# Optimization experiments

Hardware: AMD Instinct MI355X
Metric: run time of the kernel (lower is better)

Reference implementation:

```python
import jax, jax.numpy as jnp
import numpy as np

N_NODES = 100000
N_EDGES = 2500000


def setup_inputs() -> dict:
    key = jax.random.key(0)
    ks = jax.random.split(key, 6)
    x = jax.random.normal(ks[0], (N_NODES, 2), dtype=jnp.float32)
    edge_index = jax.random.randint(ks[1], (2, N_EDGES), 0, N_NODES, dtype=jnp.int32)
    # SAGEConv(2, 32): lin_l applied to mean-aggregated neighbors (carries bias),
    # lin_r applied to root features (no bias) -- PyG defaults.
    W_l1 = jax.random.normal(ks[2], (2, 32), dtype=jnp.float32) * 0.5
    W_r1 = jax.random.normal(ks[3], (2, 32), dtype=jnp.float32) * 0.5
    b1 = jnp.zeros((32,), jnp.float32)
    # SAGEConv(32, 2)
    W_l2 = jax.random.normal(ks[4], (32, 2), dtype=jnp.float32) * 0.1
    W_r2 = jax.random.normal(ks[5], (32, 2), dtype=jnp.float32) * 0.1
    b2 = jnp.zeros((2,), jnp.float32)
    return dict(x=x, edge_index=edge_index, W_l1=W_l1, W_r1=W_r1, b1=b1,
                W_l2=W_l2, W_r2=W_r2, b2=b2)


def _sage_conv(x, src, dst, deg_inv, W_l, W_r, b):
    # mean aggregation of source-node features at destination nodes
    summed = jax.ops.segment_sum(x[src], dst, num_segments=N_NODES)  # [N, F]
    agg = summed * deg_inv  # scatter-mean; isolated nodes get 0
    return agg @ W_l + x @ W_r + b


def reference(x, edge_index, W_l1, W_r1, b1, W_l2, W_r2, b2):
    src, dst = edge_index[0], edge_index[1]
    ones = jnp.ones((src.shape[0],), x.dtype)
    deg = jax.ops.segment_sum(ones, dst, num_segments=N_NODES)
    deg_inv = (1.0 / jnp.maximum(deg, 1.0))[:, None]  # [N, 1]
    h = jax.nn.relu(_sage_conv(x, src, dst, deg_inv, W_l1, W_r1, b1))
    out = _sage_conv(h, src, dst, deg_inv, W_l2, W_r2, b2)
    return jax.nn.log_softmax(out, axis=1)
```

## Files before the change

### kernel.cpp

```cpp
#include <hip/hip_runtime.h>

#define N_NODES 100000
#define N_EDGES 2500000
#define SBBITS 11
#define SBSZ 2048
#define NSB 49
#define SB 512
#define EPB 4883
#define TOT (NSB * SB)
#define P1B 25
#define M 16
#define AGG_GRID (NSB * M)


typedef unsigned int u32;
typedef unsigned long long u64;

__global__ void hist_k(const int* __restrict__ ei, u32* __restrict__ histG) {
    __shared__ u32 hl[NSB * 8];
    int t = threadIdx.x, b = blockIdx.x;
    for (int k = t; k < NSB * 8; k += 256) hl[k] = 0;
    __syncthreads();
    int e0 = b * EPB, e1 = min(e0 + EPB, N_EDGES);
    int r = t & 7;
    for (int e = e0 + t; e < e1; e += 256) {
        u32 dst = (u32)ei[N_EDGES + e];
        atomicAdd(&hl[(dst >> SBBITS) * 8 + r], 1u);
    }
    __syncthreads();
    for (int k = t; k < NSB; k += 256) {
        u32 s = 0;
#pragma unroll
        for (int j = 0; j < 8; ++j) s += hl[k * 8 + j];
        histG[k * SB + b] = s;
    }
}

__global__ void scan_p1(const u32* __restrict__ histG, u32* __restrict__ blockSum) {
    __shared__ u32 red[256];
    int t = threadIdx.x;
    int base = blockIdx.x * 1024;
    u32 s = 0;
#pragma unroll
    for (int j = 0; j < 4; ++j) {
        int idx = base + t * 4 + j;
        if (idx < TOT) s += histG[idx];
    }
    red[t] = s;
    __syncthreads();
    for (int off = 128; off > 0; off >>= 1) {
        if (t < off) red[t] += red[t + off];
        __syncthreads();
    }
    if (t == 0) blockSum[blockIdx.x] = red[0];
}

__global__ void scan_p2(const u32* __restrict__ blockSum, u32* __restrict__ blockBase) {
    __shared__ u32 ts[256];
    int t = threadIdx.x;
    u32 v[4];
    u32 s = 0;
#pragma unroll
    for (int j = 0; j < 4; ++j) {
        int idx = t * 4 + j;
        v[j] = (idx < P1B) ? blockSum[idx] : 0u;
        s += v[j];
    }
    ts[t] = s;
    __syncthreads();
    for (int off = 1; off < 256; off <<= 1) {
        u32 add = (t >= off) ? ts[t - off] : 0u;
        __syncthreads();
        ts[t] += add;
        __syncthreads();
    }
    u32 run = (t > 0) ? ts[t - 1] : 0u;
#pragma unroll
    for (int j = 0; j < 4; ++j) {
        int idx = t * 4 + j;
        if (idx < P1B) blockBase[idx] = run;
        run += v[j];
    }
}

__global__ void scan_p3(u32* histG, const u32* __restrict__ blockBase) {
    __shared__ u32 ts[256];
    int t = threadIdx.x;
    int base = blockIdx.x * 1024;
    u32 v[4];
    u32 s = 0;
#pragma unroll
    for (int j = 0; j < 4; ++j) {
        int idx = base + t * 4 + j;
        v[j] = (idx < TOT) ? histG[idx] : 0u;
        s += v[j];
    }
    ts[t] = s;
    __syncthreads();
    for (int off = 1; off < 256; off <<= 1) {
        u32 add = (t >= off) ? ts[t - off] : 0u;
        __syncthreads();
        ts[t] += add;
        __syncthreads();
    }
    u32 run = ((t > 0) ? ts[t - 1] : 0u) + blockBase[blockIdx.x];
#pragma unroll
    for (int j = 0; j < 4; ++j) {
        int idx = base + t * 4 + j;
        if (idx < TOT) histG[idx] = run;
        run += v[j];
    }
}

__global__ void scatter_k(const int* __restrict__ ei, const u32* __restrict__ histG,
                          u32* __restrict__ sortedE) {
    __shared__ u32 pos[NSB];
    int t = threadIdx.x, b = blockIdx.x;
    if (t < NSB) pos[t] = histG[t * SB + b];
    __syncthreads();
    int e0 = b * EPB, e1 = min(e0 + EPB, N_EDGES);
    for (int e = e0 + t; e < e1; e += 256) {
        u32 src = (u32)ei[e];
        u32 dst = (u32)ei[N_EDGES + e];
        u32 sb = dst >> SBBITS;
        u32 slot = atomicAdd(&pos[sb], 1u);
        sortedE[slot] = ((dst & (SBSZ - 1u)) << 17) | src;
    }
}

__global__ void agg1_k(const u32* __restrict__ sortedE, const u32* __restrict__ histG,
                       const float* __restrict__ x, u32* __restrict__ PART) {
    __shared__ u32 cntL[SBSZ], fxL[SBSZ], fyL[SBSZ];
    int t = threadIdx.x;
    u32 sb = blockIdx.x / M, m = blockIdx.x % M;
    for (int j = t; j < SBSZ; j += 256) { cntL[j] = 0; fxL[j] = 0; fyL[j] = 0; }
    __syncthreads();

    u32 s0 = histG[sb * SB];
    u32 s1 = (sb + 1 < NSB) ? histG[(sb + 1) * SB] : N_EDGES;
    u32 len = s1 - s0;
    u32 a = s0 + len * m / M;
    u32 bEnd = s0 + len * (m + 1) / M;
    const float2* x2 = (const float2*)x;

    u32 idx = a + t;
    while (idx + 256 < bEnd) {
        u32 p0 = sortedE[idx], p1 = sortedE[idx + 256];
        float2 v0 = x2[p0 & 0x1FFFFu];
        float2 v1 = x2[p1 & 0x1FFFFu];
        u32 l0 = p0 >> 17, l1 = p1 >> 17;
        atomicAdd(&cntL[l0], 1u);
        atomicAdd(&fxL[l0], (u32)((v0.x + 16.0f) * 65536.0f + 0.5f));
        atomicAdd(&fyL[l0], (u32)((v0.y + 16.0f) * 65536.0f + 0.5f));
        atomicAdd(&cntL[l1], 1u);
        atomicAdd(&fxL[l1], (u32)((v1.x + 16.0f) * 65536.0f + 0.5f));
        atomicAdd(&fyL[l1], (u32)((v1.y + 16.0f) * 65536.0f + 0.5f));
        idx += 512;
    }
    if (idx < bEnd) {
        u32 p = sortedE[idx];
        float2 v = x2[p & 0x1FFFFu];
        u32 l = p >> 17;
        atomicAdd(&cntL[l], 1u);
        atomicAdd(&fxL[l], (u32)((v.x + 16.0f) * 65536.0f + 0.5f));
        atomicAdd(&fyL[l], (u32)((v.y + 16.0f) * 65536.0f + 0.5f));
    }
    __syncthreads();

    u32 base = blockIdx.x * (3 * SBSZ);
    for (int j = t; j < SBSZ; j += 256) {
        PART[base + j] = cntL[j];
        PART[base + SBSZ + j] = fxL[j];
        PART[base + 2 * SBSZ + j] = fyL[j];
    }
}

__global__ void reduce1_node1(const u32* __restrict__ PART, const float* __restrict__ x,
                              const float* __restrict__ Wl1, const float* __restrict__ Wr1,
                              const float* __restrict__ b1,
                              const float* __restrict__ Wl2, const float* __restrict__ Wr2,
                              u64* __restrict__ ench2, float2* __restrict__ hrG,
                              float* __restrict__ degG) {
    __shared__ float sWl1[64], sWr1[64], sb1[32], sWl2[64], sWr2[64];
    int t = threadIdx.x;
    if (t < 64) { sWl1[t] = Wl1[t]; sWr1[t] = Wr1[t]; sWl2[t] = Wl2[t]; sWr2[t] = Wr2[t]; }
    if (t >= 64 && t < 96) sb1[t - 64] = b1[t - 64];
    __syncthreads();

    int i = blockIdx.x * 256 + t;
    if (i >= N_NODES) return;
    u32 sb = (u32)i >> SBBITS, j = (u32)i & (SBSZ - 1u);

    u32 cnt = 0, fx = 0, fy = 0;
#pragma unroll
    for (int m = 0; m < M; ++m) {
        u32 base = (sb * M + m) * (3 * SBSZ);
        cnt += PART[base + j];
        fx += PART[base + SBSZ + j];
        fy += PART[base + 2 * SBSZ + j];
    }

    float fc = (float)cnt;
    float dinv = 1.0f / fmaxf(fc, 1.0f);
    float ax = (float)(int)(fx - cnt * 1048576u) * (1.0f / 65536.0f) * dinv;
    float ay = (float)(int)(fy - cnt * 1048576u) * (1.0f / 65536.0f) * dinv;
    float2 xv = ((const float2*)x)[i];

    float h2a = 0.f, h2b = 0.f, hra = 0.f, hrb = 0.f;
#pragma unroll
    for (int f = 0; f < 32; ++f) {
        float h = ax * sWl1[f] + ay * sWl1[32 + f] + xv.x * sWr1[f] + xv.y * sWr1[32 + f] + sb1[f];
        h = fmaxf(h, 0.0f);
        h2a += h * sWl2[2 * f];
        h2b += h * sWl2[2 * f + 1];
        hra += h * sWr2[2 * f];
        hrb += h * sWr2[2 * f + 1];
    }
    u32 ex = (u32)((h2a + 2048.0f) * 4096.0f + 0.5f);
    u32 ey = (u32)((h2b + 2048.0f) * 4096.0f + 0.5f);
    ench2[i] = ((u64)ey << 32) | (u64)ex;
    hrG[i] = make_float2(hra, hrb);
    degG[i] = fc;
}

__global__ void agg2_k(const u32* __restrict__ sortedE, const u32* __restrict__ histG,
                       const u64* __restrict__ ench2, u32* __restrict__ PART2) {
    __shared__ u32 gxL[SBSZ], gyL[SBSZ];
    int t = threadIdx.x;
    u32 sb = blockIdx.x / M, m = blockIdx.x % M;
    for (int j = t; j < SBSZ; j += 256) { gxL[j] = 0; gyL[j] = 0; }
    __syncthreads();

    u32 s0 = histG[sb * SB];
    u32 s1 = (sb + 1 < NSB) ? histG[(sb + 1) * SB] : N_EDGES;
    u32 len = s1 - s0;
    u32 a = s0 + len * m / M;
    u32 bEnd = s0 + len * (m + 1) / M;

    u32 idx = a + t;
    while (idx + 256 < bEnd) {
        u32 p0 = sortedE[idx], p1 = sortedE[idx + 256];
        u64 e0 = ench2[p0 & 0x1FFFFu];
        u64 e1 = ench2[p1 & 0x1FFFFu];
        u32 l0 = p0 >> 17, l1 = p1 >> 17;
        atomicAdd(&gxL[l0], (u32)e0);
        atomicAdd(&gyL[l0], (u32)(e0 >> 32));
        atomicAdd(&gxL[l1], (u32)e1);
        atomicAdd(&gyL[l1], (u32)(e1 >> 32));
        idx += 512;
    }
    if (idx < bEnd) {
        u32 p = sortedE[idx];
        u64 e = ench2[p & 0x1FFFFu];
        u32 l = p >> 17;
        atomicAdd(&gxL[l], (u32)e);
        atomicAdd(&gyL[l], (u32)(e >> 32));
    }
    __syncthreads();

    u32 base = blockIdx.x * (2 * SBSZ);
    for (int j = t; j < SBSZ; j += 256) {
        PART2[base + j] = gxL[j];
        PART2[base + SBSZ + j] = gyL[j];
    }
}

__global__ void reduce2_node2(const u32* __restrict__ PART2, const float2* __restrict__ hrG,
                              const float* __restrict__ degG, const float* __restrict__ b2,
                              float* __restrict__ out) {
    int i = blockIdx.x * 256 + threadIdx.x;
    if (i >= N_NODES) return;
    u32 sb = (u32)i >> SBBITS, j = (u32)i & (SBSZ - 1u);

    u32 gx = 0, gy = 0;
#pragma unroll
    for (int m = 0; m < M; ++m) {
        u32 base = (sb * M + m) * (2 * SBSZ);
        gx += PART2[base + j];
        gy += PART2[base + SBSZ + j];
    }

    float fc = degG[i];
    u32 c = (u32)fc;
    float dinv = 1.0f / fmaxf(fc, 1.0f);
    float sx = (float)(int)(gx - c * 8388608u) * (1.0f / 4096.0f) * dinv;
    float sy = (float)(int)(gy - c * 8388608u) * (1.0f / 4096.0f) * dinv;
    float2 hv = hrG[i];
    float o0 = sx + hv.x + b2[0];
    float o1 = sy + hv.y + b2[1];
    float mx = fmaxf(o0, o1);
    float e0 = expf(o0 - mx);
    float e1 = expf(o1 - mx);
    float lse = logf(e0 + e1);
    ((float2*)out)[i] = make_float2(o0 - mx - lse, o1 - mx - lse);
}

extern "C" void kernel_launch(void* const* d_in, const int* in_sizes, int n_in,
                              void* d_out, int out_size, void* d_ws, size_t ws_size,
                              hipStream_t stream) {
    const float* x   = (const float*)d_in[0];
    const int*   ei  = (const int*)d_in[1];
    const float* Wl1 = (const float*)d_in[2];
    const float* Wr1 = (const float*)d_in[3];
    const float* b1  = (const float*)d_in[4];
    const float* Wl2 = (const float*)d_in[5];
    const float* Wr2 = (const float*)d_in[6];
    const float* b2  = (const float*)d_in[7];
    float* out = (float*)d_out;

    u32* histG     = (u32*)d_ws;
    u32* blockSum  = histG + TOT;
    u32* blockBase = blockSum + 32;
    u32* sortedE   = blockBase + 32;
    u32* PART      = sortedE + N_EDGES;
    u64* ench2     = (u64*)(PART + AGG_GRID * 3 * SBSZ);
    float2* hrG    = (float2*)(ench2 + N_NODES);
    float* degG    = (float*)(hrG + N_NODES);

    hist_k  <<<SB,  256, 0, stream>>>(ei, histG);
    scan_p1 <<<P1B, 256, 0, stream>>>(histG, blockSum);
    scan_p2 <<<1,   256, 0, stream>>>(blockSum, blockBase);
    scan_p3 <<<P1B, 256, 0, stream>>>(histG, blockBase);
    scatter_k<<<SB, 256, 0, stream>>>(ei, histG, sortedE);
    agg1_k  <<<AGG_GRID, 256, 0, stream>>>(sortedE, histG, x, PART);
    reduce1_node1<<<(N_NODES + 255) / 256, 256, 0, stream>>>(PART, x, Wl1, Wr1, b1,
                                                             Wl2, Wr2, ench2, hrG, degG);
    agg2_k  <<<AGG_GRID, 256, 0, stream>>>(sortedE, histG, ench2, PART);
    reduce2_node2<<<(N_NODES + 255) / 256, 256, 0, stream>>>(PART, hrG, degG, b2, out);
}
```

Before: 148.3 us.

## Vectorize edge loads, merge scan into single kernel, unroll aggregation loops by four

The histogram and scatter kernels now read edge indices as int4 so each thread handles four edges per load. The three-kernel prefix scan becomes one 1024-thread block that scans the whole histogram, which removes two launches and the blockSum/blockBase buffers. Both aggregation kernels unroll the gather loop to four independent loads per iteration to raise memory-level parallelism, and their tail now loops instead of handling a single leftover element. The single-block scan serialises 25 elements per thread, and the scatter output order within a bucket changes, which only affects integer-atomic accumulation order.

```diff
diff --git a/kernel.cpp b/kernel.cpp
--- a/kernel.cpp
+++ b/kernel.cpp
@@ -2,13 +2,13 @@
 
 #define N_NODES 100000
 #define N_EDGES 2500000
+#define NQ4 625000
 #define SBBITS 11
 #define SBSZ 2048
 #define NSB 49
 #define SB 512
-#define EPB 4883
+#define EPB4 1221
 #define TOT (NSB * SB)
-#define P1B 25
 #define M 16
 #define AGG_GRID (NSB * M)
 
@@ -21,11 +21,15 @@
     int t = threadIdx.x, b = blockIdx.x;
     for (int k = t; k < NSB * 8; k += 256) hl[k] = 0;
     __syncthreads();
-    int e0 = b * EPB, e1 = min(e0 + EPB, N_EDGES);
+    const int4* d4 = (const int4*)(ei + N_EDGES);
+    int q0 = b * EPB4, q1 = min(q0 + EPB4, NQ4);
     int r = t & 7;
-    for (int e = e0 + t; e < e1; e += 256) {
-        u32 dst = (u32)ei[N_EDGES + e];
-        atomicAdd(&hl[(dst >> SBBITS) * 8 + r], 1u);
+    for (int q = q0 + t; q < q1; q += 256) {
+        int4 d = d4[q];
+        atomicAdd(&hl[((u32)d.x >> SBBITS) * 8 + r], 1u);
+        atomicAdd(&hl[((u32)d.y >> SBBITS) * 8 + r], 1u);
+        atomicAdd(&hl[((u32)d.z >> SBBITS) * 8 + r], 1u);
+        atomicAdd(&hl[((u32)d.w >> SBBITS) * 8 + r], 1u);
     }
     __syncthreads();
     for (int k = t; k < NSB; k += 256) {
@@ -36,39 +40,19 @@
     }
 }
 
-__global__ void scan_p1(const u32* __restrict__ histG, u32* __restrict__ blockSum) {
-    __shared__ u32 red[256];
+__global__ void scan_all(u32* histG) {
+    __shared__ u32 ts[1024];
     int t = threadIdx.x;
-    int base = blockIdx.x * 1024;
+    int start = t * 25;
     u32 s = 0;
 #pragma unroll
-    for (int j = 0; j < 4; ++j) {
-        int idx = base + t * 4 + j;
+    for (int j = 0; j < 25; ++j) {
+        int idx = start + j;
         if (idx < TOT) s += histG[idx];
     }
-    red[t] = s;
-    __syncthreads();
-    for (int off = 128; off > 0; off >>= 1) {
-        if (t < off) red[t] += red[t + off];
-        __syncthreads();
-    }
-    if (t == 0) blockSum[blockIdx.x] = red[0];
-}
-
-__global__ void scan_p2(const u32* __restrict__ blockSum, u32* __restrict__ blockBase) {
-    __shared__ u32 ts[256];
-    int t = threadIdx.x;
-    u32 v[4];
-    u32 s = 0;
-#pragma unroll
-    for (int j = 0; j < 4; ++j) {
-        int idx = t * 4 + j;
-        v[j] = (idx < P1B) ? blockSum[idx] : 0u;
-        s += v[j];
-    }
     ts[t] = s;
     __syncthreads();
-    for (int off = 1; off < 256; off <<= 1) {
+    for (int off = 1; off < 1024; off <<= 1) {
         u32 add = (t >= off) ? ts[t - off] : 0u;
         __syncthreads();
         ts[t] += add;
@@ -76,39 +60,13 @@
     }
     u32 run = (t > 0) ? ts[t - 1] : 0u;
 #pragma unroll
-    for (int j = 0; j < 4; ++j) {
-        int idx = t * 4 + j;
-        if (idx < P1B) blockBase[idx] = run;
-        run += v[j];
-    }
-}
-
-__global__ void scan_p3(u32* histG, const u32* __restrict__ blockBase) {
-    __shared__ u32 ts[256];
-    int t = threadIdx.x;
-    int base = blockIdx.x * 1024;
-    u32 v[4];
-    u32 s = 0;
-#pragma unroll
-    for (int j = 0; j < 4; ++j) {
-        int idx = base + t * 4 + j;
-        v[j] = (idx < TOT) ? histG[idx] : 0u;
-        s += v[j];
-    }
-    ts[t] = s;
-    __syncthreads();
-    for (int off = 1; off < 256; off <<= 1) {
-        u32 add = (t >= off) ? ts[t - off] : 0u;
-        __syncthreads();
-        ts[t] += add;
-        __syncthreads();
-    }
-    u32 run = ((t > 0) ? ts[t - 1] : 0u) + blockBase[blockIdx.x];
-#pragma unroll
-    for (int j = 0; j < 4; ++j) {
-        int idx = base + t * 4 + j;
-        if (idx < TOT) histG[idx] = run;
-        run += v[j];
+    for (int j = 0; j < 25; ++j) {
+        int idx = start + j;
+        if (idx < TOT) {
+            u32 x = histG[idx];
+            histG[idx] = run;
+            run += x;
+        }
     }
 }
 
@@ -118,13 +76,21 @@
     int t = threadIdx.x, b = blockIdx.x;
     if (t < NSB) pos[t] = histG[t * SB + b];
     __syncthreads();
-    int e0 = b * EPB, e1 = min(e0 + EPB, N_EDGES);
-    for (int e = e0 + t; e < e1; e += 256) {
-        u32 src = (u32)ei[e];
-        u32 dst = (u32)ei[N_EDGES + e];
-        u32 sb = dst >> SBBITS;
-        u32 slot = atomicAdd(&pos[sb], 1u);
-        sortedE[slot] = ((dst & (SBSZ - 1u)) << 17) | src;
+    const int4* s4 = (const int4*)ei;
+    const int4* d4 = (const int4*)(ei + N_EDGES);
+    int q0 = b * EPB4, q1 = min(q0 + EPB4, NQ4);
+    for (int q = q0 + t; q < q1; q += 256) {
+        int4 sv = s4[q];
+        int4 dv = d4[q];
+        u32 slot;
+        slot = atomicAdd(&pos[(u32)dv.x >> SBBITS], 1u);
+        sortedE[slot] = (((u32)dv.x & (SBSZ - 1u)) << 17) | (u32)sv.x;
+        slot = atomicAdd(&pos[(u32)dv.y >> SBBITS], 1u);
+        sortedE[slot] = (((u32)dv.y & (SBSZ - 1u)) << 17) | (u32)sv.y;
+        slot = atomicAdd(&pos[(u32)dv.z >> SBBITS], 1u);
+        sortedE[slot] = (((u32)dv.z & (SBSZ - 1u)) << 17) | (u32)sv.z;
+        slot = atomicAdd(&pos[(u32)dv.w >> SBBITS], 1u);
+        sortedE[slot] = (((u32)dv.w & (SBSZ - 1u)) << 17) | (u32)sv.w;
     }
 }
 
@@ -144,26 +110,36 @@
     const float2* x2 = (const float2*)x;
 
     u32 idx = a + t;
-    while (idx + 256 < bEnd) {
+    while (idx + 768 < bEnd) {
         u32 p0 = sortedE[idx], p1 = sortedE[idx + 256];
+        u32 p2 = sortedE[idx + 512], p3 = sortedE[idx + 768];
         float2 v0 = x2[p0 & 0x1FFFFu];
         float2 v1 = x2[p1 & 0x1FFFFu];
-        u32 l0 = p0 >> 17, l1 = p1 >> 17;
+        float2 v2 = x2[p2 & 0x1FFFFu];
+        float2 v3 = x2[p3 & 0x1FFFFu];
+        u32 l0 = p0 >> 17, l1 = p1 >> 17, l2 = p2 >> 17, l3 = p3 >> 17;
         atomicAdd(&cntL[l0], 1u);
         atomicAdd(&fxL[l0], (u32)((v0.x + 16.0f) * 65536.0f + 0.5f));
         atomicAdd(&fyL[l0], (u32)((v0.y + 16.0f) * 65536.0f + 0.5f));
         atomicAdd(&cntL[l1], 1u);
         atomicAdd(&fxL[l1], (u32)((v1.x + 16.0f) * 65536.0f + 0.5f));
         atomicAdd(&fyL[l1], (u32)((v1.y + 16.0f) * 65536.0f + 0.5f));
-        idx += 512;
-    }
-    if (idx < bEnd) {
+        atomicAdd(&cntL[l2], 1u);
+        atomicAdd(&fxL[l2], (u32)((v2.x + 16.0f) * 65536.0f + 0.5f));
+        atomicAdd(&fyL[l2], (u32)((v2.y + 16.0f) * 65536.0f + 0.5f));
+        atomicAdd(&cntL[l3], 1u);
+        atomicAdd(&fxL[l3], (u32)((v3.x + 16.0f) * 65536.0f + 0.5f));
+        atomicAdd(&fyL[l3], (u32)((v3.y + 16.0f) * 65536.0f + 0.5f));
+        idx += 1024;
+    }
+    while (idx < bEnd) {
         u32 p = sortedE[idx];
         float2 v = x2[p & 0x1FFFFu];
         u32 l = p >> 17;
         atomicAdd(&cntL[l], 1u);
         atomicAdd(&fxL[l], (u32)((v.x + 16.0f) * 65536.0f + 0.5f));
         atomicAdd(&fyL[l], (u32)((v.y + 16.0f) * 65536.0f + 0.5f));
+        idx += 256;
     }
     __syncthreads();
 
@@ -238,23 +214,27 @@
     u32 bEnd = s0 + len * (m + 1) / M;
 
     u32 idx = a + t;
-    while (idx + 256 < bEnd) {
+    while (idx + 768 < bEnd) {
         u32 p0 = sortedE[idx], p1 = sortedE[idx + 256];
+        u32 p2 = sortedE[idx + 512], p3 = sortedE[idx + 768];
         u64 e0 = ench2[p0 & 0x1FFFFu];
         u64 e1 = ench2[p1 & 0x1FFFFu];
-        u32 l0 = p0 >> 17, l1 = p1 >> 17;
-        atomicAdd(&gxL[l0], (u32)e0);
-        atomicAdd(&gyL[l0], (u32)(e0 >> 32));
-        atomicAdd(&gxL[l1], (u32)e1);
-        atomicAdd(&gyL[l1], (u32)(e1 >> 32));
-        idx += 512;
-    }
-    if (idx < bEnd) {
+        u64 e2 = ench2[p2 & 0x1FFFFu];
+        u64 e3 = ench2[p3 & 0x1FFFFu];
+        u32 l0 = p0 >> 17, l1 = p1 >> 17, l2 = p2 >> 17, l3 = p3 >> 17;
+        atomicAdd(&gxL[l0], (u32)e0); atomicAdd(&gyL[l0], (u32)(e0 >> 32));
+        atomicAdd(&gxL[l1], (u32)e1); atomicAdd(&gyL[l1], (u32)(e1 >> 32));
+        atomicAdd(&gxL[l2], (u32)e2); atomicAdd(&gyL[l2], (u32)(e2 >> 32));
+        atomicAdd(&gxL[l3], (u32)e3); atomicAdd(&gyL[l3], (u32)(e3 >> 32));
+        idx += 1024;
+    }
+    while (idx < bEnd) {
         u32 p = sortedE[idx];
         u64 e = ench2[p & 0x1FFFFu];
         u32 l = p >> 17;
         atomicAdd(&gxL[l], (u32)e);
         atomicAdd(&gyL[l], (u32)(e >> 32));
+        idx += 256;
     }
     __syncthreads();
 
@@ -308,23 +288,19 @@
     const float* b2  = (const float*)d_in[7];
     float* out = (float*)d_out;
 
-    u32* histG     = (u32*)d_ws;
-    u32* blockSum  = histG + TOT;
-    u32* blockBase = blockSum + 32;
-    u32* sortedE   = blockBase + 32;
-    u32* PART      = sortedE + N_EDGES;
-    u64* ench2     = (u64*)(PART + AGG_GRID * 3 * SBSZ);
-    float2* hrG    = (float2*)(ench2 + N_NODES);
-    float* degG    = (float*)(hrG + N_NODES);
-
-    hist_k  <<<SB,  256, 0, stream>>>(ei, histG);
-    scan_p1 <<<P1B, 256, 0, stream>>>(histG, blockSum);
-    scan_p2 <<<1,   256, 0, stream>>>(blockSum, blockBase);
-    scan_p3 <<<P1B, 256, 0, stream>>>(histG, blockBase);
+    u32* histG   = (u32*)d_ws;
+    u32* sortedE = histG + TOT;
+    u32* PART    = sortedE + N_EDGES;
+    u64* ench2   = (u64*)(PART + AGG_GRID * 3 * SBSZ);
+    float2* hrG  = (float2*)(ench2 + N_NODES);
+    float* degG  = (float*)(hrG + N_NODES);
+
+    hist_k   <<<SB, 256, 0, stream>>>(ei, histG);
+    scan_all <<<1, 1024, 0, stream>>>(histG);
     scatter_k<<<SB, 256, 0, stream>>>(ei, histG, sortedE);
-    agg1_k  <<<AGG_GRID, 256, 0, stream>>>(sortedE, histG, x, PART);
+    agg1_k   <<<AGG_GRID, 256, 0, stream>>>(sortedE, histG, x, PART);
     reduce1_node1<<<(N_NODES + 255) / 256, 256, 0, stream>>>(PART, x, Wl1, Wr1, b1,
                                                              Wl2, Wr2, ench2, hrG, degG);
-    agg2_k  <<<AGG_GRID, 256, 0, stream>>>(sortedE, histG, ench2, PART);
+    agg2_k   <<<AGG_GRID, 256, 0, stream>>>(sortedE, histG, ench2, PART);
     reduce2_node2<<<(N_NODES + 255) / 256, 256, 0, stream>>>(PART, hrG, degG, b2, out);
 }
```

Result: slower. 171.5 us (+15.6%).
